# Performance work log

Measured on AMD Instinct MI355X. Metric: run time of the kernel, lower is better.

The kernel has to match this reference:

```python
import jax, jax.numpy as jnp
import numpy as np

B, S, D, H = 4, 2048, 1024, 16
DK = D // H

def setup_inputs() -> dict:
    key = jax.random.key(0)
    ks = jax.random.split(key, 8)
    Q = jax.random.normal(ks[0], (B, S, D), dtype=jnp.float32)
    K = jax.random.normal(ks[1], (B, S, D), dtype=jnp.float32)
    V = jax.random.normal(ks[2], (B, S, D), dtype=jnp.float32)
    # causal mask: 0 means masked (as in masked_fill(mask == 0, -inf))
    mask = jnp.broadcast_to(jnp.tril(jnp.ones((S, S), dtype=jnp.int32))[None, None], (B, 1, S, S))
    scale = 1.0 / np.sqrt(D)
    W_Q = jax.random.normal(ks[3], (D, D), dtype=jnp.float32) * scale
    W_K = jax.random.normal(ks[4], (D, D), dtype=jnp.float32) * scale
    W_V = jax.random.normal(ks[5], (D, D), dtype=jnp.float32) * scale
    W_O = jax.random.normal(ks[6], (D, D), dtype=jnp.float32) * scale
    return {"Q": Q, "K": K, "V": V, "mask": mask,
            "W_Q": W_Q, "W_K": W_K, "W_V": W_V, "W_O": W_O}

def _split_heads(x):
    # [B, S, D] -> [B, H, S, DK]
    b, s, _ = x.shape
    return x.reshape(b, s, H, DK).transpose(0, 2, 1, 3)

def reference(Q, K, V, mask, W_Q, W_K, W_V, W_O):
    # nn.Linear(d,d,bias=False): y = x @ W.T ; here W_* stored as [D, D]
    q = _split_heads(Q @ W_Q.T)
    k = _split_heads(K @ W_K.T)
    v = _split_heads(V @ W_V.T)
    scores = jnp.einsum('bhqd,bhkd->bhqk', q, k) / jnp.sqrt(jnp.float32(DK))
    scores = jnp.where(mask == 0, -jnp.inf, scores)
    weights = jax.nn.softmax(scores, axis=-1)
    weights = jnp.nan_to_num(weights, nan=0.0)  # fully-masked rows -> 0
    # dropout is identity at eval / p=0
    attn = jnp.einsum('bhqk,bhkd->bhqd', weights, v)
    attn = attn.transpose(0, 2, 1, 3).reshape(Q.shape[0], Q.shape[1], D)
    return attn @ W_O.T
```

## Files before the change

### kernel.cpp

```cpp
#include <hip/hip_runtime.h>
#include <stdint.h>

#define B_  4
#define S_  2048
#define D_  1024
#define H_  16
#define DK_ 64

typedef __attribute__((ext_vector_type(8)))  short   short8;
typedef __attribute__((ext_vector_type(8)))  unsigned short ushort8;
typedef __attribute__((ext_vector_type(4)))  float   f32x4;
typedef __attribute__((ext_vector_type(16))) float   f32x16;

#define GPTR(p) ((const __attribute__((address_space(1))) void*)(p))
#define SPTR(p) ((__attribute__((address_space(3))) void*)(p))

__device__ inline unsigned short f2bf(float f) {
  uint32_t u = __float_as_uint(f);
  uint32_t r = (u + 0x7fffu + ((u >> 16) & 1u)) >> 16;
  return (unsigned short)r;
}
__device__ inline float bf2f(unsigned short h) {
  return __uint_as_float(((uint32_t)h) << 16);
}
__device__ inline uint32_t pkbf(float a, float b) {
  uint32_t r;
  asm("v_cvt_pk_bf16_f32 %0, %1, %2" : "=v"(r) : "v"(a), "v"(b));
  return r;
}
__device__ inline void pl32(uint32_t& a, uint32_t& b) {
  asm volatile("v_permlane32_swap_b32 %0, %1" : "+v"(a), "+v"(b));
}
__device__ inline short8 mk8(uint32_t a, uint32_t b, uint32_t c, uint32_t d) {
  union { uint32_t u[4]; short8 s; } x;
  x.u[0] = a; x.u[1] = b; x.u[2] = c; x.u[3] = d;
  return x.s;
}

__global__ __launch_bounds__(256) void conv_w4(const float* __restrict__ w0,
                                               const float* __restrict__ w1,
                                               const float* __restrict__ w2,
                                               const float* __restrict__ w3,
                                               unsigned short* __restrict__ dst) {
  const size_t NW = (size_t)D_ * D_;
  const float* src = (blockIdx.z == 0) ? w0 : (blockIdx.z == 1) ? w1
                   : (blockIdx.z == 2) ? w2 : w3;
  unsigned short* d = dst + (size_t)blockIdx.z * NW;
  size_t i = ((size_t)blockIdx.x * blockDim.x + threadIdx.x) * 4;
  if (i < NW) {
    float4 v = *reinterpret_cast<const float4*>(src + i);
    ushort4 o;
    o.x = f2bf(v.x); o.y = f2bf(v.y); o.z = f2bf(v.z); o.w = f2bf(v.w);
    *reinterpret_cast<ushort4*>(d + i) = o;
  }
}

#define BM 128
#define BN 128
#define BK 32

__global__ __launch_bounds__(256) void gemm_qkv(const float* __restrict__ Xq,
                                                const float* __restrict__ Xk,
                                                const float* __restrict__ Xv,
                                                const unsigned short* __restrict__ W,
                                                unsigned short* __restrict__ P) {
  const size_t NW = (size_t)D_ * D_;
  const size_t NX = (size_t)B_ * S_ * D_;
  const int z = blockIdx.z;
  const int K = D_;

  const float* F;
  unsigned short* C;
  int N, m0, n0, f0, h0;
  if (z == 2) {
    F = Xv; C = P + 2 * NX; N = B_ * S_;
    n0 = (blockIdx.x & 63) * BN; f0 = n0;
    m0 = (blockIdx.x >> 6) * BM; h0 = m0;
  } else {
    F = z ? Xk : Xq; C = P + (size_t)z * NX; N = D_;
    m0 = (blockIdx.x & 63) * BM; f0 = m0;
    n0 = (blockIdx.x >> 6) * BN; h0 = n0;
  }
  const unsigned short* Hw = W + (size_t)z * NW;

  __shared__ float          sF[2][BM * BK];
  __shared__ unsigned short sH[2][BM * BK];

  const int tid  = threadIdx.x;
  const int lane = tid & 63;
  const int wid  = tid >> 6;
  const int wr   = wid >> 1, wc = wid & 1;
  const int g = lane >> 4, c = lane & 15;

  f32x4 acc[4][4];
#pragma unroll
  for (int m = 0; m < 4; ++m)
#pragma unroll
    for (int n = 0; n < 4; ++n) acc[m][n] = (f32x4){0.f, 0.f, 0.f, 0.f};

  auto stage = [&](int kt_, int bs) {
    const int k0 = kt_ * BK;
#pragma unroll
    for (int i = 0; i < 4; ++i) {
      const int base_ob = i * 4096 + wid * 1024;
      const int ob  = base_ob + lane * 16;
      const int row = ob >> 7;
      const int scb = (ob & 127) ^ ((row & 7) << 4);
      const float* gf = F + (size_t)(f0 + row) * K + k0 + (scb >> 2);
      __builtin_amdgcn_global_load_lds(GPTR(gf), SPTR(&sF[bs][base_ob >> 2]), 16, 0, 0);
    }
#pragma unroll
    for (int i = 0; i < 2; ++i) {
      const int base_ob = i * 4096 + wid * 1024;
      const int ob  = base_ob + lane * 16;
      const int row = ob >> 6;
      const int scb = (ob & 63) ^ (((ob >> 7) & 3) << 4);
      const unsigned short* gh = Hw + (size_t)(h0 + row) * K + k0 + (scb >> 1);
      __builtin_amdgcn_global_load_lds(GPTR(gh), SPTR(&sH[bs][base_ob >> 1]), 16, 0, 0);
    }
  };

  auto loadF = [&](const float* Fb, int r) -> short8 {
    const int b0 = r * 128 + (((g * 32)      ) ^ ((r & 7) << 4));
    const int b1 = r * 128 + (((g * 32) + 16 ) ^ ((r & 7) << 4));
    f32x4 x0 = *reinterpret_cast<const f32x4*>(
        reinterpret_cast<const char*>(Fb) + b0);
    f32x4 x1 = *reinterpret_cast<const f32x4*>(
        reinterpret_cast<const char*>(Fb) + b1);
    return mk8(pkbf(x0[0], x0[1]), pkbf(x0[2], x0[3]),
               pkbf(x1[0], x1[1]), pkbf(x1[2], x1[3]));
  };
  auto loadH = [&](const unsigned short* Hb, int r) -> short8 {
    return *reinterpret_cast<const short8*>(
        &Hb[r * BK + ((g ^ ((r >> 1) & 3)) << 3)]);
  };

  const int nkt = K / BK;
  stage(0, 0);
  for (int kt = 0; kt < nkt; ++kt) {
    const int cur = kt & 1;
    __builtin_amdgcn_s_barrier();
    __builtin_amdgcn_sched_barrier(0);
    if (kt + 1 < nkt) {
      stage(kt + 1, cur ^ 1);
      asm volatile("s_waitcnt vmcnt(6)" ::: "memory");
    } else {
      asm volatile("s_waitcnt vmcnt(0)" ::: "memory");
    }
    __builtin_amdgcn_sched_barrier(0);

    short8 af[4], bf[4];
    if (z == 2) {
#pragma unroll
      for (int m = 0; m < 4; ++m) af[m] = loadH(&sH[cur][0], wr * 64 + m * 16 + c);
#pragma unroll
      for (int n = 0; n < 4; ++n) bf[n] = loadF(&sF[cur][0], wc * 64 + n * 16 + c);
    } else {
#pragma unroll
      for (int m = 0; m < 4; ++m) af[m] = loadF(&sF[cur][0], wr * 64 + m * 16 + c);
#pragma unroll
      for (int n = 0; n < 4; ++n) bf[n] = loadH(&sH[cur][0], wc * 64 + n * 16 + c);
    }
    __builtin_amdgcn_s_setprio(1);
#pragma unroll
    for (int m = 0; m < 4; ++m)
#pragma unroll
      for (int n = 0; n < 4; ++n)
        acc[m][n] = __builtin_amdgcn_mfma_f32_16x16x32_bf16(af[m], bf[n], acc[m][n], 0, 0, 0);
    __builtin_amdgcn_s_setprio(0);
  }

#pragma unroll
  for (int m = 0; m < 4; ++m)
#pragma unroll
    for (int n = 0; n < 4; ++n)
#pragma unroll
      for (int r = 0; r < 4; ++r) {
        const int row = m0 + wr * 64 + m * 16 + 4 * g + r;
        const int col = n0 + wc * 64 + n * 16 + c;
        C[(size_t)row * N + col] = f2bf(acc[m][n][r]);
      }
}

__global__ __launch_bounds__(256) void gemm_out(const unsigned short* __restrict__ A,
                                                const unsigned short* __restrict__ Bm,
                                                float* __restrict__ C,
                                                int M, int N, int K) {
  __shared__ unsigned short sA[2][BM * BK];
  __shared__ unsigned short sB[2][BN * BK];

  const int tid  = threadIdx.x;
  const int lane = tid & 63;
  const int wid  = tid >> 6;
  const int wr   = wid >> 1, wc = wid & 1;
  const int g = lane >> 4, c = lane & 15;

  const int m0 = blockIdx.x * BM;
  const int n0 = blockIdx.y * BN;

  f32x4 acc[4][4];
#pragma unroll
  for (int m = 0; m < 4; ++m)
#pragma unroll
    for (int n = 0; n < 4; ++n) acc[m][n] = (f32x4){0.f, 0.f, 0.f, 0.f};

  auto stage = [&](int kt_, int bs) {
    const int k0 = kt_ * BK;
#pragma unroll
    for (int i = 0; i < 2; ++i) {
      const int base_ob = i * 4096 + wid * 1024;
      const int ob  = base_ob + lane * 16;
      const int row = ob >> 6;
      const int scb = (ob & 63) ^ (((ob >> 7) & 3) << 4);
      const unsigned short* ga = A  + (size_t)(m0 + row) * K + k0 + (scb >> 1);
      const unsigned short* gb = Bm + (size_t)(n0 + row) * K + k0 + (scb >> 1);
      __builtin_amdgcn_global_load_lds(GPTR(ga), SPTR(&sA[bs][base_ob >> 1]), 16, 0, 0);
      __builtin_amdgcn_global_load_lds(GPTR(gb), SPTR(&sB[bs][base_ob >> 1]), 16, 0, 0);
    }
  };

  const int nkt = K / BK;
  stage(0, 0);
  for (int kt = 0; kt < nkt; ++kt) {
    const int cur = kt & 1;
    __builtin_amdgcn_s_barrier();
    __builtin_amdgcn_sched_barrier(0);
    if (kt + 1 < nkt) {
      stage(kt + 1, cur ^ 1);
      asm volatile("s_waitcnt vmcnt(4)" ::: "memory");
    } else {
      asm volatile("s_waitcnt vmcnt(0)" ::: "memory");
    }
    __builtin_amdgcn_sched_barrier(0);

    short8 af[4], bf[4];
#pragma unroll
    for (int m = 0; m < 4; ++m) {
      const int ra = wr * 64 + m * 16 + c;
      af[m] = *reinterpret_cast<const short8*>(
          &sA[cur][ra * BK + ((g ^ ((ra >> 1) & 3)) << 3)]);
    }
#pragma unroll
    for (int n = 0; n < 4; ++n) {
      const int rb = wc * 64 + n * 16 + c;
      bf[n] = *reinterpret_cast<const short8*>(
          &sB[cur][rb * BK + ((g ^ ((rb >> 1) & 3)) << 3)]);
    }
    __builtin_amdgcn_s_setprio(1);
#pragma unroll
    for (int m = 0; m < 4; ++m)
#pragma unroll
      for (int n = 0; n < 4; ++n)
        acc[m][n] = __builtin_amdgcn_mfma_f32_16x16x32_bf16(af[m], bf[n], acc[m][n], 0, 0, 0);
    __builtin_amdgcn_s_setprio(0);
  }

#pragma unroll
  for (int m = 0; m < 4; ++m)
#pragma unroll
    for (int n = 0; n < 4; ++n)
#pragma unroll
      for (int r = 0; r < 4; ++r) {
        const int row = m0 + wr * 64 + m * 16 + 4 * g + r;
        const int col = n0 + wc * 64 + n * 16 + c;
        C[(size_t)row * N + col] = acc[m][n][r];
      }
}

__global__ __launch_bounds__(256, 4) void attn_fwd(const unsigned short* __restrict__ qp,
                                                   const unsigned short* __restrict__ kp,
                                                   const unsigned short* __restrict__ vtp,
                                                   unsigned short* __restrict__ attn) {
  const int bh = blockIdx.x;
  const int qtile = 15 - (int)blockIdx.y;
  const int b = bh >> 4, h = bh & 15;

  __shared__ unsigned short smem[4 * 64 * 64];

  const int tid  = threadIdx.x;
  const int lane = tid & 63;
  const int wid  = tid >> 6;
  const int hi   = lane >> 5;
  const int lo5  = lane & 31;

  const size_t headoff  = (size_t)b * S_ * D_ + (size_t)h * DK_;
  const size_t vheadoff = (size_t)(h * DK_) * (size_t)(B_ * S_) + (size_t)b * S_;

  const int xk = (lo5 & 7) << 4;

  auto stage = [&](int kt_, int bs) {
#pragma unroll
    for (int i = 0; i < 2; ++i) {
      const int base_ob = i * 4096 + wid * 1024;
      const int ob  = base_ob + lane * 16;
      const int row = ob >> 7;
      const int scb = (ob & 127) ^ ((row & 7) << 4);
      const unsigned short* gk = &kp[headoff + (size_t)(kt_ * 64 + row) * D_ + (scb >> 1)];
      const unsigned short* gv = &vtp[vheadoff + (size_t)row * (B_ * S_) + kt_ * 64 + (scb >> 1)];
      __builtin_amdgcn_global_load_lds(GPTR(gk), SPTR(&smem[bs * 4096 + (base_ob >> 1)]), 16, 0, 0);
      __builtin_amdgcn_global_load_lds(GPTR(gv), SPTR(&smem[8192 + bs * 4096 + (base_ob >> 1)]), 16, 0, 0);
    }
  };

  const int qw = qtile * 128 + wid * 32;
  const int qg = qw + lo5;

  short8 aq[4];
#pragma unroll
  for (int t = 0; t < 4; ++t) {
    ushort8 raw = *reinterpret_cast<const ushort8*>(
        &qp[headoff + (size_t)qg * D_ + t * 16 + hi * 8]);
    short8 sv;
#pragma unroll
    for (int j = 0; j < 8; ++j) sv[j] = (short)f2bf(bf2f(raw[j]) * 0.125f);
    aq[t] = sv;
  }

  float mrun = -3.0e38f, lrun = 0.f;
  f32x16 oa0, oa1;
#pragma unroll
  for (int r = 0; r < 16; ++r) { oa0[r] = 0.f; oa1[r] = 0.f; }

  const int nkv = 2 * (qtile + 1);
  stage(0, 0);

  for (int kt = 0; kt < nkv; ++kt) {
    const int cur = kt & 1;
    __builtin_amdgcn_s_barrier();
    __builtin_amdgcn_sched_barrier(0);
    if (kt < nkv - 1) {
      stage(kt + 1, cur ^ 1);
      asm volatile("s_waitcnt vmcnt(4)" ::: "memory");
    } else {
      asm volatile("s_waitcnt vmcnt(0)" ::: "memory");
    }
    __builtin_amdgcn_sched_barrier(0);

    const int kv0 = kt * 64;
    if (kv0 <= qw + 31) {
      const unsigned short* Kb = &smem[cur * 4096];
      const unsigned short* Vb = &smem[8192 + cur * 4096];

      f32x16 st0, st1;
#pragma unroll
      for (int r = 0; r < 16; ++r) { st0[r] = 0.f; st1[r] = 0.f; }
      __builtin_amdgcn_s_setprio(1);
#pragma unroll
      for (int t = 0; t < 4; ++t) {
        const int off = ((32 * t + 16 * hi) ^ xk) >> 1;
        short8 k0 = *reinterpret_cast<const short8*>(&Kb[lo5 * 64 + off]);
        short8 k1 = *reinterpret_cast<const short8*>(&Kb[(32 + lo5) * 64 + off]);
        st0 = __builtin_amdgcn_mfma_f32_32x32x16_bf16(k0, aq[t], st0, 0, 0, 0);
        st1 = __builtin_amdgcn_mfma_f32_32x32x16_bf16(k1, aq[t], st1, 0, 0, 0);
      }
      __builtin_amdgcn_s_setprio(0);

      if (kv0 + 63 > qw) {
#pragma unroll
        for (int r = 0; r < 16; ++r) {
          const int kvl = kv0 + (r & 3) + 8 * (r >> 2) + 4 * hi;
          if (kvl > qg)      st0[r] = -3.0e38f;
          if (kvl + 32 > qg) st1[r] = -3.0e38f;
        }
      }

      float tm = fmaxf(st0[0], st1[0]);
#pragma unroll
      for (int r = 1; r < 16; ++r) tm = fmaxf(tm, fmaxf(st0[r], st1[r]));
      tm = fmaxf(tm, __shfl_xor(tm, 32));
      const bool grow = !__all(tm <= mrun + 8.0f);
      float alpha = 1.0f;
      if (grow) {
        const float newm = fmaxf(mrun, tm);
        alpha = __expf(mrun - newm);
        mrun = newm;
      }

      float ls = 0.f;
#pragma unroll
      for (int r = 0; r < 16; ++r) { st0[r] = __expf(st0[r] - mrun); ls += st0[r]; }
      uint32_t a0 = pkbf(st0[0],  st0[1]),  a1 = pkbf(st0[2],  st0[3]);
      uint32_t b0 = pkbf(st0[4],  st0[5]),  b1 = pkbf(st0[6],  st0[7]);
      uint32_t c0 = pkbf(st0[8],  st0[9]),  c1 = pkbf(st0[10], st0[11]);
      uint32_t d0 = pkbf(st0[12], st0[13]), d1 = pkbf(st0[14], st0[15]);
      pl32(a0, b0); pl32(a1, b1);
      pl32(c0, d0); pl32(c1, d1);
      short8 pf0 = mk8(a0, a1, b0, b1);
      short8 pf1 = mk8(c0, c1, d0, d1);

#pragma unroll
      for (int r = 0; r < 16; ++r) { st1[r] = __expf(st1[r] - mrun); ls += st1[r]; }
      uint32_t e0 = pkbf(st1[0],  st1[1]),  e1 = pkbf(st1[2],  st1[3]);
      uint32_t f0 = pkbf(st1[4],  st1[5]),  f1 = pkbf(st1[6],  st1[7]);
      uint32_t g0 = pkbf(st1[8],  st1[9]),  g1 = pkbf(st1[10], st1[11]);
      uint32_t h0 = pkbf(st1[12], st1[13]), h1 = pkbf(st1[14], st1[15]);
      pl32(e0, f0); pl32(e1, f1);
      pl32(g0, h0); pl32(g1, h1);
      short8 pf2 = mk8(e0, e1, f0, f1);
      short8 pf3 = mk8(g0, g1, h0, h1);

      ls += __shfl_xor(ls, 32);
      if (grow) {
        lrun = lrun * alpha + ls;
#pragma unroll
        for (int r = 0; r < 16; ++r) { oa0[r] *= alpha; oa1[r] *= alpha; }
      } else {
        lrun += ls;
      }

      __builtin_amdgcn_s_setprio(1);
#pragma unroll
      for (int c4 = 0; c4 < 4; ++c4) {
        const int off = ((32 * c4 + 16 * hi) ^ xk) >> 1;
        short8 v0 = *reinterpret_cast<const short8*>(&Vb[lo5 * 64 + off]);
        short8 v1 = *reinterpret_cast<const short8*>(&Vb[(32 + lo5) * 64 + off]);
        const short8 pf = (c4 == 0) ? pf0 : (c4 == 1) ? pf1 : (c4 == 2) ? pf2 : pf3;
        oa0 = __builtin_amdgcn_mfma_f32_32x32x16_bf16(v0, pf, oa0, 0, 0, 0);
        oa1 = __builtin_amdgcn_mfma_f32_32x32x16_bf16(v1, pf, oa1, 0, 0, 0);
      }
      __builtin_amdgcn_s_setprio(0);
    }
  }

  __builtin_amdgcn_s_barrier();
  __builtin_amdgcn_sched_barrier(0);

  {
    unsigned short* sO = &smem[wid * (32 * 72)];
    const float inv = 1.0f / lrun;
#pragma unroll
    for (int r = 0; r < 16; ++r) {
      const int dl = (r & 3) + 8 * (r >> 2) + 4 * hi;
      sO[lo5 * 72 + dl]      = f2bf(oa0[r] * inv);
      sO[lo5 * 72 + 32 + dl] = f2bf(oa1[r] * inv);
    }
    asm volatile("s_waitcnt lgkmcnt(0)" ::: "memory");
    const int row = lane >> 1, h2 = lane & 1;
    const unsigned short* src = &smem[wid * (32 * 72) + row * 72 + h2 * 32];
    unsigned short* dst = &attn[headoff + (size_t)(qtile * 128 + wid * 32 + row) * D_ + h2 * 32];
#pragma unroll
    for (int j = 0; j < 4; ++j)
      *reinterpret_cast<short8*>(dst + 8 * j) = *reinterpret_cast<const short8*>(src + 8 * j);
  }
}

extern "C" void kernel_launch(void* const* d_in, const int* in_sizes, int n_in,
                              void* d_out, int out_size, void* d_ws, size_t ws_size,
                              hipStream_t stream) {
  const float* Q  = (const float*)d_in[0];
  const float* K  = (const float*)d_in[1];
  const float* V  = (const float*)d_in[2];
  const float* Wq = (const float*)d_in[4];
  const float* Wk = (const float*)d_in[5];
  const float* Wv = (const float*)d_in[6];
  const float* Wo = (const float*)d_in[7];
  float* out = (float*)d_out;

  const size_t NX = (size_t)B_ * S_ * D_;
  const size_t NW = (size_t)D_ * D_;

  unsigned short* ws = (unsigned short*)d_ws;
  unsigned short* Wb = ws;
  unsigned short* Pj = Wb + 4 * NW;
  unsigned short* At = Pj + 3 * NX;

  const int M = B_ * S_;
  dim3 blk(256);
  dim3 gridConvW((unsigned)(NW / 4 / 256), 1, 4);
  dim3 gridQKV(512, 1, 3);
  dim3 gridOut(M / BM, D_ / BN);
  dim3 gridAttn(B_ * H_, 16);

  conv_w4<<<gridConvW, blk, 0, stream>>>(Wq, Wk, Wv, Wo, Wb);
  gemm_qkv<<<gridQKV, blk, 0, stream>>>(Q, K, V, Wb, Pj);
  attn_fwd<<<gridAttn, blk, 0, stream>>>(Pj, Pj + NX, Pj + 2 * NX, At);
  gemm_out<<<gridOut, blk, 0, stream>>>(At, Wb + 3 * NW, out, M, D_, D_);
}
```

Baseline: 174.1 us.

## Stage fp32 activations through registers and store bf16 tiles in LDS

The QKV projection GEMM no longer copies fp32 activation tiles straight into LDS and converts them to bf16 on every fragment read. Each thread now loads its fp32 activations into registers two k-tiles ahead, converts them to bf16 once, and writes them into a bf16 LDS buffer with the same swizzle as the weight tile. This halves LDS space and traffic for activations and removes repeated conversions across waves. The cost is more registers held across iterations, more complex vmcnt/lgkmcnt bookkeeping, and LDS writes from VGPRs instead of asynchronous direct-to-LDS loads.

```diff
diff --git a/kernel.cpp b/kernel.cpp
--- a/kernel.cpp
+++ b/kernel.cpp
@@ -83,7 +83,7 @@
   }
   const unsigned short* Hw = W + (size_t)z * NW;
 
-  __shared__ float          sF[2][BM * BK];
+  __shared__ unsigned short sF[2][BM * BK];
   __shared__ unsigned short sH[2][BM * BK];
 
   const int tid  = threadIdx.x;
@@ -91,6 +91,8 @@
   const int wid  = tid >> 6;
   const int wr   = wid >> 1, wc = wid & 1;
   const int g = lane >> 4, c = lane & 15;
+  const int fr = tid >> 3;
+  const int fq = tid & 7;
 
   f32x4 acc[4][4];
 #pragma unroll
@@ -98,17 +100,8 @@
 #pragma unroll
     for (int n = 0; n < 4; ++n) acc[m][n] = (f32x4){0.f, 0.f, 0.f, 0.f};
 
-  auto stage = [&](int kt_, int bs) {
+  auto stageH = [&](int kt_, int bs) {
     const int k0 = kt_ * BK;
-#pragma unroll
-    for (int i = 0; i < 4; ++i) {
-      const int base_ob = i * 4096 + wid * 1024;
-      const int ob  = base_ob + lane * 16;
-      const int row = ob >> 7;
-      const int scb = (ob & 127) ^ ((row & 7) << 4);
-      const float* gf = F + (size_t)(f0 + row) * K + k0 + (scb >> 2);
-      __builtin_amdgcn_global_load_lds(GPTR(gf), SPTR(&sF[bs][base_ob >> 2]), 16, 0, 0);
-    }
 #pragma unroll
     for (int i = 0; i < 2; ++i) {
       const int base_ob = i * 4096 + wid * 1024;
@@ -120,46 +113,72 @@
     }
   };
 
-  auto loadF = [&](const float* Fb, int r) -> short8 {
-    const int b0 = r * 128 + (((g * 32)      ) ^ ((r & 7) << 4));
-    const int b1 = r * 128 + (((g * 32) + 16 ) ^ ((r & 7) << 4));
-    f32x4 x0 = *reinterpret_cast<const f32x4*>(
-        reinterpret_cast<const char*>(Fb) + b0);
-    f32x4 x1 = *reinterpret_cast<const f32x4*>(
-        reinterpret_cast<const char*>(Fb) + b1);
-    return mk8(pkbf(x0[0], x0[1]), pkbf(x0[2], x0[3]),
-               pkbf(x1[0], x1[1]), pkbf(x1[2], x1[3]));
+  float4 fA0, fA1, fA2, fA3, fB0, fB1, fB2, fB3;
+  auto loadFreg = [&](float4& s0, float4& s1, float4& s2, float4& s3, int kt_) {
+    const float* p = F + (size_t)(f0 + fr) * K + kt_ * BK + fq * 4;
+    s0 = *reinterpret_cast<const float4*>(p);
+    s1 = *reinterpret_cast<const float4*>(p + (size_t)32 * K);
+    s2 = *reinterpret_cast<const float4*>(p + (size_t)64 * K);
+    s3 = *reinterpret_cast<const float4*>(p + (size_t)96 * K);
   };
-  auto loadH = [&](const unsigned short* Hb, int r) -> short8 {
+  auto writeF = [&](const float4& s0, const float4& s1, const float4& s2,
+                    const float4& s3, int bs) {
+    const int sl   = (fq >> 1) ^ ((fr >> 1) & 3);
+    const int off0 = fr * 32 + (sl << 3) + (fq & 1) * 4;
+    uint2 w0; w0.x = pkbf(s0.x, s0.y); w0.y = pkbf(s0.z, s0.w);
+    uint2 w1; w1.x = pkbf(s1.x, s1.y); w1.y = pkbf(s1.z, s1.w);
+    uint2 w2; w2.x = pkbf(s2.x, s2.y); w2.y = pkbf(s2.z, s2.w);
+    uint2 w3; w3.x = pkbf(s3.x, s3.y); w3.y = pkbf(s3.z, s3.w);
+    *reinterpret_cast<uint2*>(&sF[bs][off0])            = w0;
+    *reinterpret_cast<uint2*>(&sF[bs][off0 + 32 * 32])  = w1;
+    *reinterpret_cast<uint2*>(&sF[bs][off0 + 64 * 32])  = w2;
+    *reinterpret_cast<uint2*>(&sF[bs][off0 + 96 * 32])  = w3;
+  };
+  auto frag = [&](const unsigned short* Tb, int r) -> short8 {
     return *reinterpret_cast<const short8*>(
-        &Hb[r * BK + ((g ^ ((r >> 1) & 3)) << 3)]);
+        &Tb[r * BK + ((g ^ ((r >> 1) & 3)) << 3)]);
   };
 
   const int nkt = K / BK;
-  stage(0, 0);
+  loadFreg(fA0, fA1, fA2, fA3, 0);
+  stageH(0, 0);
+  asm volatile("s_waitcnt vmcnt(0)" ::: "memory");
+  writeF(fA0, fA1, fA2, fA3, 0);
+  loadFreg(fB0, fB1, fB2, fB3, 1);
+  asm volatile("s_waitcnt lgkmcnt(0)" ::: "memory");
+
   for (int kt = 0; kt < nkt; ++kt) {
     const int cur = kt & 1;
     __builtin_amdgcn_s_barrier();
     __builtin_amdgcn_sched_barrier(0);
-    if (kt + 1 < nkt) {
-      stage(kt + 1, cur ^ 1);
-      asm volatile("s_waitcnt vmcnt(6)" ::: "memory");
-    } else {
-      asm volatile("s_waitcnt vmcnt(0)" ::: "memory");
-    }
-    __builtin_amdgcn_sched_barrier(0);
+    const bool issueH = (kt + 1 < nkt);
+    const bool issueF = (kt + 2 < nkt);
+    if (issueH) stageH(kt + 1, cur ^ 1);
+    if (issueF) {
+      if (kt & 1) { loadFreg(fB0, fB1, fB2, fB3, kt + 2); }
+      else        { loadFreg(fA0, fA1, fA2, fA3, kt + 2); }
+    }
+    if (issueF)      { asm volatile("s_waitcnt vmcnt(6)" ::: "memory"); }
+    else if (issueH) { asm volatile("s_waitcnt vmcnt(2)" ::: "memory"); }
+    else             { asm volatile("s_waitcnt vmcnt(0)" ::: "memory"); }
+    __builtin_amdgcn_sched_barrier(0);
+
+    if (issueH) {
+      if (kt & 1) { writeF(fA0, fA1, fA2, fA3, cur ^ 1); }
+      else        { writeF(fB0, fB1, fB2, fB3, cur ^ 1); }
+    }
 
     short8 af[4], bf[4];
     if (z == 2) {
 #pragma unroll
-      for (int m = 0; m < 4; ++m) af[m] = loadH(&sH[cur][0], wr * 64 + m * 16 + c);
-#pragma unroll
-      for (int n = 0; n < 4; ++n) bf[n] = loadF(&sF[cur][0], wc * 64 + n * 16 + c);
+      for (int m = 0; m < 4; ++m) af[m] = frag(&sH[cur][0], wr * 64 + m * 16 + c);
+#pragma unroll
+      for (int n = 0; n < 4; ++n) bf[n] = frag(&sF[cur][0], wc * 64 + n * 16 + c);
     } else {
 #pragma unroll
-      for (int m = 0; m < 4; ++m) af[m] = loadF(&sF[cur][0], wr * 64 + m * 16 + c);
-#pragma unroll
-      for (int n = 0; n < 4; ++n) bf[n] = loadH(&sH[cur][0], wc * 64 + n * 16 + c);
+      for (int m = 0; m < 4; ++m) af[m] = frag(&sF[cur][0], wr * 64 + m * 16 + c);
+#pragma unroll
+      for (int n = 0; n < 4; ++n) bf[n] = frag(&sH[cur][0], wc * 64 + n * 16 + c);
     }
     __builtin_amdgcn_s_setprio(1);
 #pragma unroll
@@ -168,6 +187,9 @@
       for (int n = 0; n < 4; ++n)
         acc[m][n] = __builtin_amdgcn_mfma_f32_16x16x32_bf16(af[m], bf[n], acc[m][n], 0, 0, 0);
     __builtin_amdgcn_s_setprio(0);
+
+    asm volatile("s_waitcnt lgkmcnt(0)" ::: "memory");
+    __builtin_amdgcn_sched_barrier(0);
   }
 
 #pragma unroll
```

New measurement: 177.6 us. 1.02x slower.
